# Kernel tuning notes

Measured on AMD Instinct MI355X. Metric: run time of the kernel, lower is better.

## Reference

```python
import jax, jax.numpy as jnp
import numpy as np
import math

MU = 5; ETA = 1.0; ITERS = 3
SIGMA_C = 1.0; SIGMA_S = 1.6 * SIGMA_C
SIGMA_M = 3.0; RHO = 0.99; TAU = 0.7
MAX_T = int(math.floor(3 * SIGMA_C))  # 3
MAX_S = int(math.floor(3 * SIGMA_M))  # 9
DELTA = 1.0
B, C, X, Y = 4, 1, 512, 512


def _gpdf(v, sig):
    return math.exp(-v * v / (2.0 * sig * sig)) / (math.sqrt(2.0 * math.pi) * sig)


def _sobel(img):
    k = jnp.array([[-1., -2., -1.], [0., 0., 0.], [1., 2., 1.]], dtype=img.dtype)
    kern = jnp.stack([k, k.T])[:, None]  # [2,1,3,3] OIHW
    return jax.lax.conv_general_dilated(img, kern, (1, 1), [(1, 1), (1, 1)],
                                        dimension_numbers=('NCHW', 'OIHW', 'NCHW'))


def _gather_flat(arr, idx):
    # arr [b,c,x,y], idx int [b,x,y] flattened spatial index (px*Y+py)
    b, c, x, y = arr.shape
    flat = arr.reshape(b, c, x * y)
    idxb = jnp.broadcast_to(idx.reshape(b, 1, x * y), (b, c, x * y))
    return jnp.take_along_axis(flat, idxb, axis=2).reshape(b, c, x, y)


def _safe_norm(v):
    m = jnp.linalg.norm(v, axis=1, keepdims=True)
    return v / jnp.where(m == 0, 1.0, m)


def _etf(images):
    b, c, x, y = images.shape
    sob = _sobel(images)                                   # [b,2,x,y]
    mag = jnp.linalg.norm(sob, axis=1, keepdims=True)      # [b,1,x,y]
    mag = mag / jnp.max(mag)
    mag_p = jnp.pad(mag, ((0, 0), (0, 0), (MU, MU), (MU, MU)))
    sobel_X = mag[:, None]                                 # [b,1,1,x,y]
    tang = _safe_norm(jnp.stack([-sob[:, 1], sob[:, 0]], axis=1))
    K = 2 * MU + 1
    for _ in range(ITERS):
        for ori in ('V', 'H'):
            tang_p = jnp.pad(tang, ((0, 0), (0, 0), (MU, MU), (MU, MU)))
            tang_X = tang[:, None]                         # [b,1,2,x,y]
            if ori == 'V':
                tang_Y = jnp.stack([tang_p[:, :, i:i + x, MU:MU + y] for i in range(K)], axis=1)
                sobel_Y = jnp.stack([mag_p[:, :, i:i + x, MU:MU + y] for i in range(K)], axis=1)
            else:
                tang_Y = jnp.stack([tang_p[:, :, MU:MU + x, i:i + y] for i in range(K)], axis=1)
                sobel_Y = jnp.stack([mag_p[:, :, MU:MU + x, i:i + y] for i in range(K)], axis=1)
            # weight: magnitude term * direction term / 2
            w = (jnp.tanh(ETA * (sobel_Y - sobel_X)) + 1.0) \
                * jnp.sum(tang_X * tang_Y, axis=2, keepdims=True) * 0.5
            tang = _safe_norm(jnp.sum(tang_Y * w, axis=1))
    return tang


def _dog(images, etf):
    b, c, x, y = images.shape
    xi, yi = jnp.meshgrid(jnp.arange(x, dtype=images.dtype),
                          jnp.arange(y, dtype=images.dtype), indexing='ij')
    idx0 = jnp.broadcast_to(jnp.stack([xi, yi])[None], (b, 2, x, y))
    per = jnp.stack([-etf[:, 1], etf[:, 0]], axis=1)       # perpendicular to flow
    dog = jnp.zeros_like(images)
    tw = 0.0
    for t in range(-MAX_T, MAX_T + 1):
        pts = idx0 + DELTA * per * t
        px = jnp.round(jnp.clip(pts[:, 0], 0, x - 1)).astype(jnp.int32)
        py = jnp.round(jnp.clip(pts[:, 1], 0, y - 1)).astype(jnp.int32)
        il = _gather_flat(images, px * y + py)
        gw = _gpdf(t, SIGMA_C) - RHO * _gpdf(t, SIGMA_S)
        tw += gw
        dog = dog + il * gw
    return dog / tw


def _fdog_float(images):
    b, c, x, y = images.shape
    etf = _etf(images)
    dog = _dog(images, etf)
    fdog = jnp.zeros_like(images)
    tw = 0.0
    xi, yi = jnp.meshgrid(jnp.arange(x, dtype=jnp.int32),
                          jnp.arange(y, dtype=jnp.int32), indexing='ij')
    for s_dir in (-1, 1):
        px = jnp.broadcast_to(xi[None], (b, x, y))
        py = jnp.broadcast_to(yi[None], (b, x, y))
        for s in range(0 if s_dir == 1 else 1, MAX_S + 1):
            if s != 0:
                p_etf = _gather_flat(etf, px * y + py)     # flow at current points
                fx = px.astype(images.dtype) + DELTA * p_etf[:, 0] * s_dir
                fy = py.astype(images.dtype) + DELTA * p_etf[:, 1] * s_dir
                px = jnp.round(jnp.clip(fx, 0, x - 1)).astype(jnp.int32)
                py = jnp.round(jnp.clip(fy, 0, y - 1)).astype(jnp.int32)
            f_s = _gather_flat(dog, px * y + py)
            gw = _gpdf(s, SIGMA_M)
            tw += gw
            fdog = fdog + f_s * gw
    return fdog / tw


def setup_inputs() -> dict:
    key = jax.random.key(0)
    images = jax.random.uniform(key, (B, C, X, Y), dtype=jnp.float32)
    return {"images": images}


def reference(images):
    fdog = _fdog_float(images)
    edges = ~((fdog < 0) & (1.0 + jnp.tanh(fdog) < TAU))
    return edges.astype(jnp.int32)
```

## Files before the change

kernel.cpp:

```cpp
#include <hip/hip_runtime.h>
#include <math.h>

#pragma clang fp contract(off)

#define BN 4
#define SX 512
#define SY 512
#define NPIX (BN * SX * SY)
#define MU 5
#define MB (1024 * 1024)
#define NBLOCKS 4096

struct DogW  { float g[7];  float tw; };
struct FdogW { float g[10]; float tw; };

__device__ __forceinline__ float fast_tanh_f32(float dF) {
    double d = (double)dF;
    double y = fabs(d);
    double t = expm1(2.0 * y);
    double r = t / (t + 2.0);
    if (y > 350.0) r = 1.0;
    return (float)copysign(r, d);
}

__device__ __forceinline__ float img_at(const float* __restrict__ img, int b, int x, int y) {
    if (x < 0 || x >= SX || y < 0 || y >= SY) return 0.0f;
    return img[(size_t)b * SX * SY + (size_t)x * SY + y];
}

__global__ void k_sobel(const float* __restrict__ img, float* __restrict__ mag,
                        float2* __restrict__ tang, float* __restrict__ partial) {
#pragma clang fp contract(off)
    int yi = blockIdx.x * blockDim.x + threadIdx.x;
    int xi = blockIdx.y;
    int b  = blockIdx.z;

    float v00 = img_at(img, b, xi - 1, yi - 1);
    float v01 = img_at(img, b, xi - 1, yi    );
    float v02 = img_at(img, b, xi - 1, yi + 1);
    float v10 = img_at(img, b, xi,     yi - 1);
    float v12 = img_at(img, b, xi,     yi + 1);
    float v20 = img_at(img, b, xi + 1, yi - 1);
    float v21 = img_at(img, b, xi + 1, yi    );
    float v22 = img_at(img, b, xi + 1, yi + 1);

    float s0 = (-1.0f * v00);
    s0 = s0 + (-2.0f * v01);
    s0 = s0 + (-1.0f * v02);
    s0 = s0 + ( 1.0f * v20);
    s0 = s0 + ( 2.0f * v21);
    s0 = s0 + ( 1.0f * v22);
    float s1 = (-1.0f * v00);
    s1 = s1 + ( 1.0f * v02);
    s1 = s1 + (-2.0f * v10);
    s1 = s1 + ( 2.0f * v12);
    s1 = s1 + (-1.0f * v20);
    s1 = s1 + ( 1.0f * v22);

    float m = sqrtf((s0 * s0) + (s1 * s1));
    size_t idx = (size_t)b * SX * SY + (size_t)xi * SY + yi;
    mag[idx] = m;

    float tx = -s1, ty = s0;
    float n = sqrtf((tx * tx) + (ty * ty));
    float d = (n == 0.0f) ? 1.0f : n;
    tang[idx] = make_float2(tx / d, ty / d);

    float wm = m;
    for (int off = 32; off > 0; off >>= 1) wm = fmaxf(wm, __shfl_down(wm, off, 64));
    __shared__ float red[4];
    int lane = threadIdx.x & 63;
    int wid  = threadIdx.x >> 6;
    if (lane == 0) red[wid] = wm;
    __syncthreads();
    if (threadIdx.x == 0) {
        float bm = fmaxf(fmaxf(red[0], red[1]), fmaxf(red[2], red[3]));
        int bid = blockIdx.x + gridDim.x * (blockIdx.y + gridDim.y * blockIdx.z);
        partial[bid] = bm;
    }
}

__global__ void k_reduce(const float* __restrict__ partial, unsigned int* __restrict__ maxbits) {
    float m = 0.0f;
    for (int i = threadIdx.x; i < NBLOCKS; i += 256) m = fmaxf(m, partial[i]);
    for (int off = 32; off > 0; off >>= 1) m = fmaxf(m, __shfl_down(m, off, 64));
    __shared__ float red[4];
    int lane = threadIdx.x & 63;
    int wid  = threadIdx.x >> 6;
    if (lane == 0) red[wid] = m;
    __syncthreads();
    if (threadIdx.x == 0) {
        float bm = fmaxf(fmaxf(red[0], red[1]), fmaxf(red[2], red[3]));
        *maxbits = __float_as_uint(bm);
    }
}

__global__ void k_norm(float* __restrict__ mag, const unsigned int* __restrict__ maxbits) {
    int i = blockIdx.x * blockDim.x + threadIdx.x;
    float mx = __uint_as_float(*maxbits);
    mag[i] = mag[i] / mx;
}

__global__ void k_tanh(const float* __restrict__ mag, const unsigned int* __restrict__ maxbits,
                       float* __restrict__ TV, float* __restrict__ TH) {
#pragma clang fp contract(off)
    int yi = blockIdx.x * blockDim.x + threadIdx.x;
    int xi = blockIdx.y;
    int b  = blockIdx.z;
    size_t base = (size_t)b * SX * SY;
    size_t idx  = base + (size_t)xi * SY + yi;
    float mx = __uint_as_float(*maxbits);
    float cm = mag[idx] / mx;
#pragma unroll
    for (int k = 1; k <= 5; ++k) {
        if (xi + k < SX) {
            float nm = mag[idx + (size_t)k * SY] / mx;
            TV[(size_t)(k - 1) * NPIX + idx] = fast_tanh_f32(nm - cm);
        }
    }
#pragma unroll
    for (int k = 1; k <= 5; ++k) {
        if (yi + k < SY) {
            float nm = mag[idx + k] / mx;
            TH[(size_t)(k - 1) * NPIX + idx] = fast_tanh_f32(nm - cm);
        }
    }
}

#define VTY 32
#define VTX 8
__global__ __launch_bounds__(256) void k_etf_v(const float2* __restrict__ tsrc,
                                               float2* __restrict__ tdst,
                                               const float* __restrict__ TV) {
#pragma clang fp contract(off)
    int ty = threadIdx.x;
    int tx = threadIdx.y;
    int y0 = blockIdx.x * VTY;
    int x0 = blockIdx.y * VTX;
    int b  = blockIdx.z;
    int yi = y0 + ty;
    int xi = x0 + tx;
    size_t base = (size_t)b * SX * SY;
    size_t idx  = base + (size_t)xi * SY + yi;

    __shared__ float2 sT[VTX + 2 * MU][VTY];
    for (int r = tx; r < VTX + 2 * MU; r += VTX) {
        int gx = x0 - MU + r;
        if (gx >= 0 && gx < SX)
            sT[r][ty] = tsrc[base + (size_t)gx * SY + yi];
    }
    __syncthreads();

    float2 ct = sT[tx + MU][ty];

    float sx = 0.0f, sy = 0.0f;
#pragma unroll
    for (int k = -MU; k <= MU; ++k) {
        int nx = xi + k;
        if (nx < 0 || nx >= SX) continue;
        float2 nt = sT[tx + MU + k][ty];
        float th;
        if (k > 0)      th =  TV[(size_t)(k - 1) * NPIX + idx];
        else if (k < 0) th = -TV[(size_t)(-k - 1) * NPIX + (idx + (size_t)k * SY)];
        else            th =  0.0f;
        float dot = (ct.x * nt.x) + (ct.y * nt.y);
        float w   = ((th + 1.0f) * dot) * 0.5f;
        sx = sx + (nt.x * w);
        sy = sy + (nt.y * w);
    }
    float n = sqrtf((sx * sx) + (sy * sy));
    float d = (n == 0.0f) ? 1.0f : n;
    tdst[idx] = make_float2(sx / d, sy / d);
}

__global__ void k_etf_h(const float2* __restrict__ tsrc, float2* __restrict__ tdst,
                        const float* __restrict__ TH) {
#pragma clang fp contract(off)
    int yi = blockIdx.x * blockDim.x + threadIdx.x;
    int xi = blockIdx.y;
    int b  = blockIdx.z;
    size_t base = (size_t)b * SX * SY;
    size_t idx  = base + (size_t)xi * SY + yi;

    float2 ct = tsrc[idx];

    float sx = 0.0f, sy = 0.0f;
#pragma unroll
    for (int k = -MU; k <= MU; ++k) {
        int ny = yi + k;
        if (ny < 0 || ny >= SY) continue;
        size_t nidx = idx + k;
        float2 nt = tsrc[nidx];
        float th;
        if (k > 0)      th =  TH[(size_t)(k - 1) * NPIX + idx];
        else if (k < 0) th = -TH[(size_t)(-k - 1) * NPIX + nidx];
        else            th =  0.0f;
        float dot = (ct.x * nt.x) + (ct.y * nt.y);
        float w   = ((th + 1.0f) * dot) * 0.5f;
        sx = sx + (nt.x * w);
        sy = sy + (nt.y * w);
    }
    float n = sqrtf((sx * sx) + (sy * sy));
    float d = (n == 0.0f) ? 1.0f : n;
    tdst[idx] = make_float2(sx / d, sy / d);
}

__global__ void k_etf(const float2* __restrict__ tsrc, float2* __restrict__ tdst,
                      const float* __restrict__ mag, int vert) {
#pragma clang fp contract(off)
    int yi = blockIdx.x * blockDim.x + threadIdx.x;
    int xi = blockIdx.y;
    int b  = blockIdx.z;
    size_t base = (size_t)b * SX * SY;
    size_t idx  = base + (size_t)xi * SY + yi;

    float  cm = mag[idx];
    float2 ct = tsrc[idx];

    float sx = 0.0f, sy = 0.0f;
    for (int k = -MU; k <= MU; ++k) {
        int nx = xi + (vert ? k : 0);
        int ny = yi + (vert ? 0 : k);
        if (nx < 0 || nx >= SX || ny < 0 || ny >= SY) continue;
        size_t nidx = base + (size_t)nx * SY + ny;
        float  nm = mag[nidx];
        float2 nt = tsrc[nidx];
        float dot = (ct.x * nt.x) + (ct.y * nt.y);
        float th  = (float)tanh((double)(nm - cm));
        float w   = ((th + 1.0f) * dot) * 0.5f;
        sx = sx + (nt.x * w);
        sy = sy + (nt.y * w);
    }
    float n = sqrtf((sx * sx) + (sy * sy));
    float d = (n == 0.0f) ? 1.0f : n;
    tdst[idx] = make_float2(sx / d, sy / d);
}

__global__ void k_dog(const float* __restrict__ img, const float2* __restrict__ etf,
                      float* __restrict__ dog, DogW w) {
#pragma clang fp contract(off)
    int yi = blockIdx.x * blockDim.x + threadIdx.x;
    int xi = blockIdx.y;
    int b  = blockIdx.z;
    size_t base = (size_t)b * SX * SY;
    size_t idx  = base + (size_t)xi * SY + yi;

    float2 e = etf[idx];
    float perx = -e.y;
    float pery =  e.x;
    float xf = (float)xi, yf = (float)yi;

    float acc = 0.0f;
#pragma unroll
    for (int t = -3; t <= 3; ++t) {
        float tf  = (float)t;
        float ptx = xf + (perx * tf);
        float pty = yf + (pery * tf);
        int px = (int)rintf(fminf(fmaxf(ptx, 0.0f), (float)(SX - 1)));
        int py = (int)rintf(fminf(fmaxf(pty, 0.0f), (float)(SY - 1)));
        float il = img[base + (size_t)px * SY + py];
        acc = acc + (il * w.g[t + 3]);
    }
    dog[idx] = acc / w.tw;
}

__global__ void k_fdog(const float* __restrict__ dog, const float2* __restrict__ etf,
                       int* __restrict__ out, FdogW w) {
#pragma clang fp contract(off)
    int yi = blockIdx.x * blockDim.x + threadIdx.x;
    int xi = blockIdx.y;
    int b  = blockIdx.z;
    size_t base = (size_t)b * SX * SY;
    size_t idx  = base + (size_t)xi * SY + yi;

    float acc = 0.0f;

    int px = xi, py = yi;
    for (int s = 1; s <= 9; ++s) {
        float2 e = etf[base + (size_t)px * SY + py];
        float fx = (float)px + (e.x * -1.0f);
        float fy = (float)py + (e.y * -1.0f);
        px = (int)rintf(fminf(fmaxf(fx, 0.0f), (float)(SX - 1)));
        py = (int)rintf(fminf(fmaxf(fy, 0.0f), (float)(SY - 1)));
        acc = acc + (dog[base + (size_t)px * SY + py] * w.g[s]);
    }

    px = xi; py = yi;
    acc = acc + (dog[base + (size_t)px * SY + py] * w.g[0]);
    for (int s = 1; s <= 9; ++s) {
        float2 e = etf[base + (size_t)px * SY + py];
        float fx = (float)px + (e.x * 1.0f);
        float fy = (float)py + (e.y * 1.0f);
        px = (int)rintf(fminf(fmaxf(fx, 0.0f), (float)(SX - 1)));
        py = (int)rintf(fminf(fmaxf(fy, 0.0f), (float)(SY - 1)));
        acc = acc + (dog[base + (size_t)px * SY + py] * w.g[s]);
    }

    float fv = acc / w.tw;
    float th = 1.0f + fast_tanh_f32(fv);
    out[idx] = ((fv < 0.0f) && (th < 0.7f)) ? 0 : 1;
}

static double gpdf(double v, double sig) {
    return exp(-(v * v) / (2.0 * sig * sig)) / (sqrt(2.0 * M_PI) * sig);
}

extern "C" void kernel_launch(void* const* d_in, const int* in_sizes, int n_in,
                              void* d_out, int out_size, void* d_ws, size_t ws_size,
                              hipStream_t stream) {
    const float* img = (const float*)d_in[0];
    int* out = (int*)d_out;
    char* ws = (char*)d_ws;

    const size_t need = (size_t)60 * MB + NBLOCKS * sizeof(float) + 4;
    bool fast = ws_size >= need;

    float*  mag = (float*)(ws);
    float2* tA  = (float2*)(ws + (size_t)4  * MB);
    float2* tB  = (float2*)(ws + (size_t)12 * MB);
    float*  dog = (float*)(ws + (size_t)12 * MB);
    float*  TV  = (float*)(ws + (size_t)20 * MB);
    float*  TH  = (float*)(ws + (size_t)40 * MB);
    size_t  tail = fast ? (size_t)60 * MB : (size_t)20 * MB;
    float*        partial = (float*)(ws + tail);
    unsigned int* maxbits = (unsigned int*)(ws + tail + NBLOCKS * sizeof(float));

    dim3 blk(256, 1, 1);
    dim3 grd(SY / 256, SX, BN);
    dim3 vblk(VTY, VTX, 1);
    dim3 vgrd(SY / VTY, SX / VTX, BN);

    k_sobel<<<grd, blk, 0, stream>>>(img, mag, tA, partial);
    k_reduce<<<1, 256, 0, stream>>>(partial, maxbits);

    float2* src = tA;
    float2* dst = tB;
    if (fast) {
        k_tanh<<<grd, blk, 0, stream>>>(mag, maxbits, TV, TH);
        for (int it = 0; it < 3; ++it) {
            k_etf_v<<<vgrd, vblk, 0, stream>>>(src, dst, TV);
            { float2* t = src; src = dst; dst = t; }
            k_etf_h<<<grd, blk, 0, stream>>>(src, dst, TH);
            { float2* t = src; src = dst; dst = t; }
        }
    } else {
        k_norm<<<NPIX / 256, 256, 0, stream>>>(mag, maxbits);
        for (int it = 0; it < 3; ++it) {
            k_etf<<<grd, blk, 0, stream>>>(src, dst, mag, 1);
            { float2* t = src; src = dst; dst = t; }
            k_etf<<<grd, blk, 0, stream>>>(src, dst, mag, 0);
            { float2* t = src; src = dst; dst = t; }
        }
    }
    float* dogbuf = (src == tA) ? dog : (float*)tA;

    DogW dw;
    {
        double tw = 0.0;
        for (int t = -3; t <= 3; ++t) {
            double g = gpdf((double)t, 1.0) - 0.99 * gpdf((double)t, 1.6);
            dw.g[t + 3] = (float)g;
            tw += g;
        }
        dw.tw = (float)tw;
    }
    k_dog<<<grd, blk, 0, stream>>>(img, src, dogbuf, dw);

    FdogW fw;
    {
        for (int s = 0; s <= 9; ++s) fw.g[s] = (float)gpdf((double)s, 3.0);
        double tw = 0.0;
        for (int s = 1; s <= 9; ++s) tw += gpdf((double)s, 3.0);
        for (int s = 0; s <= 9; ++s) tw += gpdf((double)s, 3.0);
        fw.tw = (float)tw;
    }
    k_fdog<<<grd, blk, 0, stream>>>(dogbuf, src, out, fw);
}
```

Measured before the change: 203.1 us.

## Stage ETF tiles and tanh tables in LDS with vector loads; interleave FDoG walks

```diff
diff --git a/kernel.cpp b/kernel.cpp
--- a/kernel.cpp
+++ b/kernel.cpp
@@ -133,23 +133,42 @@
                                                float2* __restrict__ tdst,
                                                const float* __restrict__ TV) {
 #pragma clang fp contract(off)
-    int ty = threadIdx.x;
-    int tx = threadIdx.y;
+    int ty = threadIdx.x & 31;
+    int tx = threadIdx.x >> 5;
     int y0 = blockIdx.x * VTY;
     int x0 = blockIdx.y * VTX;
     int b  = blockIdx.z;
-    int yi = y0 + ty;
-    int xi = x0 + tx;
     size_t base = (size_t)b * SX * SY;
-    size_t idx  = base + (size_t)xi * SY + yi;
-
-    __shared__ float2 sT[VTX + 2 * MU][VTY];
-    for (int r = tx; r < VTX + 2 * MU; r += VTX) {
+
+    __shared__ __align__(16) float2 sT[VTX + 2 * MU][VTY];
+    __shared__ __align__(16) float  sTV[5][VTX + MU][VTY];
+
+    int tid = threadIdx.x;
+    for (int i = tid; i < (VTX + 2 * MU) * (VTY / 2) / 2; i += 256) {
+        break;
+    }
+    for (int i = tid; i < (VTX + 2 * MU) * (VTY / 4) * 2; i += 256) {
+        int r = i >> 4;
+        int c = i & 15;
         int gx = x0 - MU + r;
         if (gx >= 0 && gx < SX)
-            sT[r][ty] = tsrc[base + (size_t)gx * SY + yi];
+            ((float4*)&sT[r][0])[c] = ((const float4*)(tsrc + base + (size_t)gx * SY + y0))[c];
+    }
+    for (int i = tid; i < 5 * (VTX + MU) * (VTY / 4); i += 256) {
+        int j   = i / ((VTX + MU) * (VTY / 4));
+        int rem = i - j * ((VTX + MU) * (VTY / 4));
+        int r   = rem >> 3;
+        int c   = rem & 7;
+        int gx  = x0 - MU + r;
+        if (gx >= 0 && gx < SX)
+            ((float4*)&sTV[j][r][0])[c] =
+                ((const float4*)(TV + (size_t)j * NPIX + base + (size_t)gx * SY + y0))[c];
     }
     __syncthreads();
+
+    int xi = x0 + tx;
+    int yi = y0 + ty;
+    size_t idx = base + (size_t)xi * SY + yi;
 
     float2 ct = sT[tx + MU][ty];
 
@@ -160,8 +179,8 @@
         if (nx < 0 || nx >= SX) continue;
         float2 nt = sT[tx + MU + k][ty];
         float th;
-        if (k > 0)      th =  TV[(size_t)(k - 1) * NPIX + idx];
-        else if (k < 0) th = -TV[(size_t)(-k - 1) * NPIX + (idx + (size_t)k * SY)];
+        if (k > 0)      th =  sTV[k - 1][tx + MU][ty];
+        else if (k < 0) th = -sTV[-k - 1][tx + MU + k][ty];
         else            th =  0.0f;
         float dot = (ct.x * nt.x) + (ct.y * nt.y);
         float w   = ((th + 1.0f) * dot) * 0.5f;
@@ -173,36 +192,49 @@
     tdst[idx] = make_float2(sx / d, sy / d);
 }
 
-__global__ void k_etf_h(const float2* __restrict__ tsrc, float2* __restrict__ tdst,
-                        const float* __restrict__ TH) {
-#pragma clang fp contract(off)
-    int yi = blockIdx.x * blockDim.x + threadIdx.x;
-    int xi = blockIdx.y;
-    int b  = blockIdx.z;
-    size_t base = (size_t)b * SX * SY;
-    size_t idx  = base + (size_t)xi * SY + yi;
-
-    float2 ct = tsrc[idx];
-
-    float sx = 0.0f, sy = 0.0f;
-#pragma unroll
-    for (int k = -MU; k <= MU; ++k) {
-        int ny = yi + k;
-        if (ny < 0 || ny >= SY) continue;
-        size_t nidx = idx + k;
-        float2 nt = tsrc[nidx];
-        float th;
-        if (k > 0)      th =  TH[(size_t)(k - 1) * NPIX + idx];
-        else if (k < 0) th = -TH[(size_t)(-k - 1) * NPIX + nidx];
-        else            th =  0.0f;
-        float dot = (ct.x * nt.x) + (ct.y * nt.y);
-        float w   = ((th + 1.0f) * dot) * 0.5f;
-        sx = sx + (nt.x * w);
-        sy = sy + (nt.y * w);
-    }
-    float n = sqrtf((sx * sx) + (sy * sy));
-    float d = (n == 0.0f) ? 1.0f : n;
-    tdst[idx] = make_float2(sx / d, sy / d);
+__global__ __launch_bounds__(256) void k_etf_h(const float2* __restrict__ tsrc,
+                                               float2* __restrict__ tdst,
+                                               const float* __restrict__ TH) {
+#pragma clang fp contract(off)
+    int tid = threadIdx.x;
+    int xi  = blockIdx.y;
+    int b   = blockIdx.z;
+    size_t rowbase = (size_t)b * SX * SY + (size_t)xi * SY;
+
+    __shared__ __align__(16) float2 sT[SY];
+    __shared__ __align__(16) float  sTH[5][SY];
+
+    ((float4*)sT)[tid] = ((const float4*)(tsrc + rowbase))[tid];
+    for (int i = tid; i < 5 * (SY / 4); i += 256) {
+        int j = i >> 7;
+        int c = i & 127;
+        ((float4*)&sTH[0][0])[i] = ((const float4*)(TH + (size_t)j * NPIX + rowbase))[c];
+    }
+    __syncthreads();
+
+#pragma unroll
+    for (int half = 0; half < 2; ++half) {
+        int yi = tid + half * 256;
+        float2 ct = sT[yi];
+        float sx = 0.0f, sy = 0.0f;
+#pragma unroll
+        for (int k = -MU; k <= MU; ++k) {
+            int ny = yi + k;
+            if (ny < 0 || ny >= SY) continue;
+            float2 nt = sT[ny];
+            float th;
+            if (k > 0)      th =  sTH[k - 1][yi];
+            else if (k < 0) th = -sTH[-k - 1][ny];
+            else            th =  0.0f;
+            float dot = (ct.x * nt.x) + (ct.y * nt.y);
+            float w   = ((th + 1.0f) * dot) * 0.5f;
+            sx = sx + (nt.x * w);
+            sy = sy + (nt.y * w);
+        }
+        float n = sqrtf((sx * sx) + (sy * sy));
+        float d = (n == 0.0f) ? 1.0f : n;
+        tdst[rowbase + yi] = make_float2(sx / d, sy / d);
+    }
 }
 
 __global__ void k_etf(const float2* __restrict__ tsrc, float2* __restrict__ tdst,
@@ -273,28 +305,41 @@
     size_t base = (size_t)b * SX * SY;
     size_t idx  = base + (size_t)xi * SY + yi;
 
+    float d1[9];
+    float d2[10];
+    float2 e0 = etf[idx];
+    float2 e1 = e0, e2 = e0;
+    int p1x = xi, p1y = yi;
+    int p2x = xi, p2y = yi;
+    d2[0] = dog[idx];
+
+#pragma unroll
+    for (int s = 1; s <= 9; ++s) {
+        float fx1 = (float)p1x + (e1.x * -1.0f);
+        float fy1 = (float)p1y + (e1.y * -1.0f);
+        p1x = (int)rintf(fminf(fmaxf(fx1, 0.0f), (float)(SX - 1)));
+        p1y = (int)rintf(fminf(fmaxf(fy1, 0.0f), (float)(SY - 1)));
+        size_t i1 = base + (size_t)p1x * SY + p1y;
+        float fx2 = (float)p2x + (e2.x * 1.0f);
+        float fy2 = (float)p2y + (e2.y * 1.0f);
+        p2x = (int)rintf(fminf(fmaxf(fx2, 0.0f), (float)(SX - 1)));
+        p2y = (int)rintf(fminf(fmaxf(fy2, 0.0f), (float)(SY - 1)));
+        size_t i2 = base + (size_t)p2x * SY + p2y;
+
+        d1[s - 1] = dog[i1];
+        d2[s]     = dog[i2];
+        if (s < 9) {
+            e1 = etf[i1];
+            e2 = etf[i2];
+        }
+    }
+
     float acc = 0.0f;
-
-    int px = xi, py = yi;
-    for (int s = 1; s <= 9; ++s) {
-        float2 e = etf[base + (size_t)px * SY + py];
-        float fx = (float)px + (e.x * -1.0f);
-        float fy = (float)py + (e.y * -1.0f);
-        px = (int)rintf(fminf(fmaxf(fx, 0.0f), (float)(SX - 1)));
-        py = (int)rintf(fminf(fmaxf(fy, 0.0f), (float)(SY - 1)));
-        acc = acc + (dog[base + (size_t)px * SY + py] * w.g[s]);
-    }
-
-    px = xi; py = yi;
-    acc = acc + (dog[base + (size_t)px * SY + py] * w.g[0]);
-    for (int s = 1; s <= 9; ++s) {
-        float2 e = etf[base + (size_t)px * SY + py];
-        float fx = (float)px + (e.x * 1.0f);
-        float fy = (float)py + (e.y * 1.0f);
-        px = (int)rintf(fminf(fmaxf(fx, 0.0f), (float)(SX - 1)));
-        py = (int)rintf(fminf(fmaxf(fy, 0.0f), (float)(SY - 1)));
-        acc = acc + (dog[base + (size_t)px * SY + py] * w.g[s]);
-    }
+#pragma unroll
+    for (int s = 1; s <= 9; ++s) acc = acc + (d1[s - 1] * w.g[s]);
+    acc = acc + (d2[0] * w.g[0]);
+#pragma unroll
+    for (int s = 1; s <= 9; ++s) acc = acc + (d2[s] * w.g[s]);
 
     float fv = acc / w.tw;
     float th = 1.0f + fast_tanh_f32(fv);
@@ -327,8 +372,8 @@
 
     dim3 blk(256, 1, 1);
     dim3 grd(SY / 256, SX, BN);
-    dim3 vblk(VTY, VTX, 1);
     dim3 vgrd(SY / VTY, SX / VTX, BN);
+    dim3 hgrd(1, SX, BN);
 
     k_sobel<<<grd, blk, 0, stream>>>(img, mag, tA, partial);
     k_reduce<<<1, 256, 0, stream>>>(partial, maxbits);
@@ -338,9 +383,9 @@
     if (fast) {
         k_tanh<<<grd, blk, 0, stream>>>(mag, maxbits, TV, TH);
         for (int it = 0; it < 3; ++it) {
-            k_etf_v<<<vgrd, vblk, 0, stream>>>(src, dst, TV);
+            k_etf_v<<<vgrd, blk, 0, stream>>>(src, dst, TV);
             { float2* t = src; src = dst; dst = t; }
-            k_etf_h<<<grd, blk, 0, stream>>>(src, dst, TH);
+            k_etf_h<<<hgrd, blk, 0, stream>>>(src, dst, TH);
             { float2* t = src; src = dst; dst = t; }
         }
     } else {
```

New measurement: 195.6 us. 1.04x faster.
